# Kernel tuning notes

Measured on AMD Instinct MI355X. Metric: run time of the kernel, lower is better.

## Reference

```python
import jax, jax.numpy as jnp
import numpy as np

D = 64       # embedding_dim
N = 10000    # nodes
E = 160000   # edges (avg degree 16)
R = 16       # removals
C = 512      # connected edges scored per removal


def setup_inputs() -> dict:
    key = jax.random.key(0)
    ks = jax.random.split(key, 18)
    coords = jax.random.normal(ks[0], (N, 2), jnp.float32)
    edge_src = jax.random.randint(ks[1], (E,), 0, N, jnp.int32)
    edge_dst = jax.random.randint(ks[2], (E,), 0, N, jnp.int32)
    removal_idx = jax.random.randint(ks[3], (R,), 0, N, jnp.int32)
    conn_eidx = jax.random.randint(ks[4], (R, C), 0, E, jnp.int32)
    s2 = 1.0 / np.sqrt(2.0)
    sD = 1.0 / np.sqrt(D)
    s2D = 1.0 / np.sqrt(2 * D)
    return {
        "coords": coords,
        "W_emb": jax.random.normal(ks[5], (2, D), jnp.float32) * s2,
        "b_emb": jnp.zeros((D,), jnp.float32),
        "W_self0": jax.random.normal(ks[6], (D, D), jnp.float32) * sD,
        "W_neigh0": jax.random.normal(ks[7], (D, D), jnp.float32) * sD,
        "b_gnn0": jnp.zeros((D,), jnp.float32),
        "W_self1": jax.random.normal(ks[8], (D, D), jnp.float32) * sD,
        "W_neigh1": jax.random.normal(ks[9], (D, D), jnp.float32) * sD,
        "b_gnn1": jnp.zeros((D,), jnp.float32),
        "W_edge": jax.random.normal(ks[10], (2 * D, D), jnp.float32) * s2D,
        "b_edge": jnp.zeros((D,), jnp.float32),
        "W_score": jax.random.normal(ks[11], (2 * D, 1), jnp.float32) * s2D,
        "b_score": jnp.zeros((1,), jnp.float32),
        "edge_src": edge_src,
        "edge_dst": edge_dst,
        "removal_idx": removal_idx,
        "conn_eidx": conn_eidx,
    }


def reference(coords, W_emb, b_emb, W_self0, W_neigh0, b_gnn0,
              W_self1, W_neigh1, b_gnn1, W_edge, b_edge, W_score, b_score,
              edge_src, edge_dst, removal_idx, conn_eidx):
    Nn = coords.shape[0]
    h0 = coords @ W_emb + b_emb  # [N, D] init node embedding

    def gnn_layer(h, emask, Ws, Wn, b):
        # masked mean aggregation of neighbor messages, then linear + relu
        msg = h[edge_src] * emask[:, None]                       # [E, D]
        agg = jax.ops.segment_sum(msg, edge_dst, num_segments=Nn)
        deg = jax.ops.segment_sum(emask, edge_dst, num_segments=Nn)
        agg = agg / jnp.maximum(deg, 1.0)[:, None]
        return jax.nn.relu(h @ Ws + agg @ Wn + b)

    def per_removal(r, conn):
        # tempDestroy: mask out removed node's participation in message passing
        nmask = jnp.ones((Nn,), coords.dtype).at[r].set(0.0)
        emask = nmask[edge_src] * nmask[edge_dst]                # [E]
        h = h0
        h = gnn_layer(h, emask, W_self0, W_neigh0, b_gnn0) + h   # residual
        h = gnn_layer(h, emask, W_self1, W_neigh1, b_gnn1) + h
        s, d = edge_src[conn], edge_dst[conn]                    # connected edges
        ef = jax.nn.relu(jnp.concatenate([h[s], h[d]], -1) @ W_edge + b_edge)  # [C, D]
        r_embed = coords[r] @ W_emb + b_emb                      # [D]
        score_in = jnp.concatenate(
            [jnp.broadcast_to(r_embed, (conn.shape[0], r_embed.shape[0])), ef], -1)
        score = score_in @ W_score + b_score                     # [C, 1]
        return jax.nn.softmax(score, axis=0)[:, 0]               # softmax over edges

    return jax.vmap(per_removal)(removal_idx, conn_eidx)         # [R, C]
```

## Files before the change

### kernel.cpp

```cpp
#include <hip/hip_runtime.h>

#define Df 64
#define NN 10000
#define EE 160000
#define RR 16
#define CC 512
#define CAP1 128
#define CAP2 2048
#define BST 128
#define NGEMM 157
#define NAGG 2500
#define NEDG 625
#define NSLF 40
#define ND1B 512
#define ND2B 8192

__device__ float g_h0[NN * Df];
__device__ float g_h1b[NN * Df];
__device__ float g_h2b[NN * Df];
__device__ float g_agg[NN * Df];
__device__ float g_zrow[Df];
__device__ __align__(16) float g_W20[128 * Df];
__device__ __align__(16) float g_W21[128 * Df];
__device__ int g_deg[NN];
__device__ __align__(16) int g_bkt[NN * BST];
__device__ int g_m1mask[NN], g_m2mask[NN];
__device__ int g_mark1[RR][NN], g_mark2[RR][NN];
__device__ int g_n1[RR], g_n2[RR];
__device__ int g_list1[RR][CAP1], g_list2[RR][CAP2];
__device__ float g_d1[RR][CAP1][Df];
__device__ float g_d2[RR][CAP2][Df];
__device__ float g_score[RR * CC];

__device__ void compact256(const int* __restrict__ maskArr, int bit,
                           int* mark, int* list, int* nout, int cap) {
    int t = threadIdx.x;
    int lane = t & 63, wv = t >> 6;
    const int PER = 40;
    int base = t * PER;
    int loc = 0;
    for (int k = 0; k < PER; k++) { int v = base + k; if (v < NN) loc += (maskArr[v] >> bit) & 1; }
    int sc = loc;
#pragma unroll
    for (int off = 1; off < 64; off <<= 1) { int x = __shfl_up(sc, off, 64); if (lane >= off) sc += x; }
    __shared__ int wsumC[4];
    if (lane == 63) wsumC[wv] = sc;
    __syncthreads();
    if (t == 0) { int a = 0; for (int w2 = 0; w2 < 4; w2++) { int x = wsumC[w2]; wsumC[w2] = a; a += x; } }
    __syncthreads();
    int run = wsumC[wv] + (sc - loc);
    for (int k = 0; k < PER; k++) {
        int v = base + k;
        if (v < NN) {
            int f = (maskArr[v] >> bit) & 1;
            if (f && run < cap) { list[run] = v; mark[v] = run + 1; }
            else mark[v] = 0;
            run += f;
        }
    }
    if (t == 255) *nout = (run < cap) ? run : cap;
    __syncthreads();
}

__device__ void agg8(const float* __restrict__ hin, int b, int tid) {
    int lane = tid & 63, w = tid >> 6;
    int n = b * 4 + w;
    int deg = g_deg[n];
    int dg = deg < BST ? deg : BST;
    const int* bp = &g_bkt[n * BST];
    float s0 = 0.f, s1 = 0.f, s2 = 0.f, s3 = 0.f;
    float s4 = 0.f, s5 = 0.f, s6 = 0.f, s7 = 0.f;
    int i = 0;
    for (; i + 8 <= dg; i += 8) {
        int4 a = *(const int4*)&bp[i];
        int4 c = *(const int4*)&bp[i + 4];
        s0 += hin[a.x * Df + lane];
        s1 += hin[a.y * Df + lane];
        s2 += hin[a.z * Df + lane];
        s3 += hin[a.w * Df + lane];
        s4 += hin[c.x * Df + lane];
        s5 += hin[c.y * Df + lane];
        s6 += hin[c.z * Df + lane];
        s7 += hin[c.w * Df + lane];
    }
    for (; i < dg; i++) s0 += hin[bp[i] * Df + lane];
    float s = ((s0 + s1) + (s2 + s3)) + ((s4 + s5) + (s6 + s7));
    g_agg[n * Df + lane] = s / fmaxf((float)deg, 1.f);
}

__device__ void gemm_tile(const float* __restrict__ hin, float* __restrict__ hout,
                          const float* __restrict__ W2, const float* __restrict__ bias,
                          int m0, int tid, char* smem) {
    float (*Xs)[68] = (float(*)[68])smem;
    float (*Wl)[64] = (float(*)[64])(smem + 8704);
    int tx = tid & 15, ty = tid >> 4;
    float acc[4][4];
#pragma unroll
    for (int i = 0; i < 4; i++)
#pragma unroll
        for (int j = 0; j < 4; j++) acc[i][j] = 0.f;

    for (int c = 0; c < 4; c++) {
        const float* src = (c < 2) ? hin : g_agg;
        int kb = (c & 1) * 32;
        int kbase = c * 32;
#pragma unroll
        for (int rep = 0; rep < 2; rep++) {
            int slot = tid + rep * 256;
            int m = slot >> 3, q = slot & 7;
            int n = m0 + m;
            float4 v = make_float4(0.f, 0.f, 0.f, 0.f);
            if (n < NN) v = *(const float4*)&src[n * Df + kb + q * 4];
            Xs[q * 4 + 0][m] = v.x; Xs[q * 4 + 1][m] = v.y;
            Xs[q * 4 + 2][m] = v.z; Xs[q * 4 + 3][m] = v.w;
            int k = slot >> 4, dq = slot & 15;
            *(float4*)&Wl[k][dq * 4] = *(const float4*)&W2[(kbase + k) * Df + dq * 4];
        }
        __syncthreads();
#pragma unroll
        for (int k = 0; k < 32; k++) {
            float4 x4 = *(const float4*)&Xs[k][ty * 4];
            float4 w4 = *(const float4*)&Wl[k][tx * 4];
            float xs[4] = {x4.x, x4.y, x4.z, x4.w};
            float ws[4] = {w4.x, w4.y, w4.z, w4.w};
#pragma unroll
            for (int i = 0; i < 4; i++)
#pragma unroll
                for (int j = 0; j < 4; j++) acc[i][j] += xs[i] * ws[j];
        }
        __syncthreads();
    }
    float4 b4 = *(const float4*)&bias[tx * 4];
    float bb[4] = {b4.x, b4.y, b4.z, b4.w};
#pragma unroll
    for (int i = 0; i < 4; i++) {
        int n = m0 + ty * 4 + i;
        if (n < NN) {
            float4 hv = *(const float4*)&hin[n * Df + tx * 4];
            float4 o;
            o.x = fmaxf(acc[i][0] + bb[0], 0.f) + hv.x;
            o.y = fmaxf(acc[i][1] + bb[1], 0.f) + hv.y;
            o.z = fmaxf(acc[i][2] + bb[2], 0.f) + hv.z;
            o.w = fmaxf(acc[i][3] + bb[3], 0.f) + hv.w;
            *(float4*)&hout[n * Df + tx * 4] = o;
        }
    }
}

__device__ void delta1_blk(int rel, int tid, const int* __restrict__ removal,
                           const float* __restrict__ Ws, const float* __restrict__ Wn,
                           const float* __restrict__ bias, char* smem) {
    float* s_h = (float*)smem;
    float* s_a = s_h + 4 * Df;
    int ri = rel >> 5, y = rel & 31;
    int lane = tid & 63, w = tid >> 6;
    int j = y * 4 + w;
    if (j >= g_n1[ri]) return;
    int v = g_list1[ri][j];
    int r = removal[ri];
    float p0s = 0.f, p1s = 0.f, p2s = 0.f, p3s = 0.f; int cnt = 0;
    if (v != r) {
        int deg = g_deg[v];
        int dg = deg < BST ? deg : BST;
        const int* bp = &g_bkt[v * BST];
        int i = 0;
        for (; i + 4 <= dg; i += 4) {
            int c0 = bp[i], c1 = bp[i + 1], c2 = bp[i + 2], c3 = bp[i + 3];
            const float* p0 = (c0 == r) ? g_zrow : &g_h0[c0 * Df];
            const float* p1 = (c1 == r) ? g_zrow : &g_h0[c1 * Df];
            const float* p2 = (c2 == r) ? g_zrow : &g_h0[c2 * Df];
            const float* p3 = (c3 == r) ? g_zrow : &g_h0[c3 * Df];
            p0s += p0[lane]; p1s += p1[lane]; p2s += p2[lane]; p3s += p3[lane];
            cnt += (c0 != r) + (c1 != r) + (c2 != r) + (c3 != r);
        }
        for (; i < dg; i++) {
            int c = bp[i];
            const float* p = (c == r) ? g_zrow : &g_h0[c * Df];
            p0s += p[lane]; cnt += (c != r);
        }
    }
    float aggd = (p0s + p1s) + (p2s + p3s);
    float hv = g_h0[v * Df + lane];
    s_h[w * Df + lane] = hv;
    s_a[w * Df + lane] = aggd / fmaxf((float)cnt, 1.f);
    float acc = bias[lane];
#pragma unroll 16
    for (int k = 0; k < Df; k++)
        acc += s_h[w * Df + k] * Ws[k * Df + lane] + s_a[w * Df + k] * Wn[k * Df + lane];
    g_d1[ri][j][lane] = fmaxf(acc, 0.f) + hv;
}

__device__ void delta2_blk(int rel, int tid, const int* __restrict__ removal,
                           const float* __restrict__ Ws, const float* __restrict__ Wn,
                           const float* __restrict__ bias, char* smem) {
    float* s_h = (float*)smem;
    float* s_a = s_h + 4 * Df;
    int ri = rel >> 9, y = rel & 511;
    int lane = tid & 63, w = tid >> 6;
    int j = y * 4 + w;
    if (j >= g_n2[ri]) return;
    int v = g_list2[ri][j];
    int r = removal[ri];
    const int* mk1 = g_mark1[ri];
    float p0s = 0.f, p1s = 0.f, p2s = 0.f, p3s = 0.f; int cnt = 0;
    if (v != r) {
        int deg = g_deg[v];
        int dg = deg < BST ? deg : BST;
        const int* bp = &g_bkt[v * BST];
        int i = 0;
        for (; i + 4 <= dg; i += 4) {
            int c0 = bp[i], c1 = bp[i + 1], c2 = bp[i + 2], c3 = bp[i + 3];
            int m0 = mk1[c0], m1 = mk1[c1], m2 = mk1[c2], m3 = mk1[c3];
            const float* p0 = (c0 == r) ? g_zrow : (m0 > 0 ? &g_d1[ri][m0 - 1][0] : &g_h1b[c0 * Df]);
            const float* p1 = (c1 == r) ? g_zrow : (m1 > 0 ? &g_d1[ri][m1 - 1][0] : &g_h1b[c1 * Df]);
            const float* p2 = (c2 == r) ? g_zrow : (m2 > 0 ? &g_d1[ri][m2 - 1][0] : &g_h1b[c2 * Df]);
            const float* p3 = (c3 == r) ? g_zrow : (m3 > 0 ? &g_d1[ri][m3 - 1][0] : &g_h1b[c3 * Df]);
            p0s += p0[lane]; p1s += p1[lane]; p2s += p2[lane]; p3s += p3[lane];
            cnt += (c0 != r) + (c1 != r) + (c2 != r) + (c3 != r);
        }
        for (; i < dg; i++) {
            int c = bp[i];
            int m = mk1[c];
            const float* p = (c == r) ? g_zrow : (m > 0 ? &g_d1[ri][m - 1][0] : &g_h1b[c * Df]);
            p0s += p[lane]; cnt += (c != r);
        }
    }
    float aggd = (p0s + p1s) + (p2s + p3s);
    int mv = mk1[v];
    float hv = (mv > 0) ? g_d1[ri][mv - 1][lane] : g_h1b[v * Df + lane];
    s_h[w * Df + lane] = hv;
    s_a[w * Df + lane] = aggd / fmaxf((float)cnt, 1.f);
    float acc = bias[lane];
#pragma unroll 16
    for (int k = 0; k < Df; k++)
        acc += s_h[w * Df + k] * Ws[k * Df + lane] + s_a[w * Df + k] * Wn[k * Df + lane];
    g_d2[ri][j][lane] = fmaxf(acc, 0.f) + hv;
}

__global__ void k_init(const float* __restrict__ coords, const float* __restrict__ We,
                       const float* __restrict__ be, const float* __restrict__ Ws0,
                       const float* __restrict__ Wn0, const float* __restrict__ Ws1,
                       const float* __restrict__ Wn1) {
    int i = blockIdx.x * 256 + threadIdx.x;
    if (i < NN * Df) {
        int n = i >> 6, d = i & 63;
        g_h0[i] = coords[2 * n] * We[d] + coords[2 * n + 1] * We[Df + d] + be[d];
    }
    if (i < NN) { g_deg[i] = 0; g_m1mask[i] = 0; g_m2mask[i] = 0; }
    if (i < Df) g_zrow[i] = 0.f;
    if (i < 8192) {
        int k = i >> 6, d = i & 63;
        g_W20[i] = (k < 64) ? Ws0[k * 64 + d] : Wn0[(k - 64) * 64 + d];
        g_W21[i] = (k < 64) ? Ws1[k * 64 + d] : Wn1[(k - 64) * 64 + d];
    }
}

__global__ void k_fillflag(const int* __restrict__ esrc, const int* __restrict__ edst,
                           const int* __restrict__ removal) {
    __shared__ int s_rem[RR];
    int tid = threadIdx.x;
    if (tid < RR) s_rem[tid] = removal[tid];
    __syncthreads();
    int e = blockIdx.x * 256 + tid;
    if (e < EE) {
        int s = esrc[e], d = edst[e];
        int p = atomicAdd(&g_deg[d], 1);
        if (p < BST) g_bkt[d * BST + p] = s;
        int m = 0;
#pragma unroll
        for (int ri = 0; ri < RR; ri++)
            if (s == s_rem[ri]) m |= (1 << ri);
        if (m) atomicOr(&g_m1mask[d], m);
    }
    if (blockIdx.x == 0 && tid < RR)
        atomicOr(&g_m1mask[removal[tid]], 1 << tid);
}

__global__ __launch_bounds__(256) void k_L3(const int* __restrict__ esrc,
                                            const int* __restrict__ edst) {
    int b = blockIdx.x, tid = threadIdx.x;
    if (b < NAGG) { agg8(g_h0, b, tid); return; }
    if (b < NAGG + NEDG) {
        int e = (b - NAGG) * 256 + tid;
        if (e < EE) {
            int m = g_m1mask[esrc[e]];
            if (m) atomicOr(&g_m2mask[edst[e]], m);
        }
        return;
    }
    if (b < NAGG + NEDG + NSLF) {
        int v = (b - NAGG - NEDG) * 256 + tid;
        if (v < NN) {
            int m = g_m1mask[v];
            if (m) atomicOr(&g_m2mask[v], m);
        }
        return;
    }
    int ri = b - NAGG - NEDG - NSLF;
    compact256(g_m1mask, ri, g_mark1[ri], g_list1[ri], &g_n1[ri], CAP1);
}

__global__ __launch_bounds__(256) void k_L4(const int* __restrict__ removal,
        const float* __restrict__ Ws0, const float* __restrict__ Wn0,
        const float* __restrict__ b0) {
    __shared__ __align__(16) char smem[16896];
    int b = blockIdx.x, tid = threadIdx.x;
    if (b < NGEMM) { gemm_tile(g_h0, g_h1b, g_W20, b0, b * 64, tid, smem); return; }
    if (b < NGEMM + ND1B) { delta1_blk(b - NGEMM, tid, removal, Ws0, Wn0, b0, smem); return; }
    int ri = b - NGEMM - ND1B;
    compact256(g_m2mask, ri, g_mark2[ri], g_list2[ri], &g_n2[ri], CAP2);
}

__global__ __launch_bounds__(256) void k_L5(const int* __restrict__ removal,
        const float* __restrict__ Ws1, const float* __restrict__ Wn1,
        const float* __restrict__ b1) {
    __shared__ __align__(16) char smem[2048];
    int b = blockIdx.x, tid = threadIdx.x;
    if (b < NAGG) { agg8(g_h1b, b, tid); return; }
    delta2_blk(b - NAGG, tid, removal, Ws1, Wn1, b1, smem);
}

__global__ __launch_bounds__(256) void k_gemm1(const float* __restrict__ b1) {
    __shared__ __align__(16) char smem[16896];
    gemm_tile(g_h1b, g_h2b, g_W21, b1, blockIdx.x * 64, threadIdx.x, smem);
}

__global__ __launch_bounds__(256) void k_score(const int* __restrict__ conn,
        const int* __restrict__ removal, const int* __restrict__ esrc,
        const int* __restrict__ edst, const float* __restrict__ We,
        const float* __restrict__ be, const float* __restrict__ Wsc,
        const float* __restrict__ bsc) {
    __shared__ const float* ptrs[128];
    __shared__ float Xs[32][68];
    __shared__ float Wl[32][64];
    __shared__ float su;
    int tid = threadIdx.x;
    int e0 = blockIdx.x * 64;
    int ri = e0 >> 9;

    if (tid < 64) {
        int e = conn[e0 + tid];
        int s = esrc[e], d = edst[e];
        int ms = g_mark2[ri][s], md = g_mark2[ri][d];
        ptrs[tid]      = (ms > 0) ? &g_d2[ri][ms - 1][0] : &g_h2b[s * Df];
        ptrs[64 + tid] = (md > 0) ? &g_d2[ri][md - 1][0] : &g_h2b[d * Df];
    } else if (tid < 128) {
        int lane = tid & 63;
        float up = g_h0[removal[ri] * Df + lane] * Wsc[lane];
#pragma unroll
        for (int off = 32; off > 0; off >>= 1) up += __shfl_xor(up, off, 64);
        if (lane == 0) su = up;
    }
    __syncthreads();

    int tx = tid & 15, ty = tid >> 4;
    float acc[4][4];
#pragma unroll
    for (int i = 0; i < 4; i++)
#pragma unroll
        for (int j = 0; j < 4; j++) acc[i][j] = 0.f;

    for (int c = 0; c < 4; c++) {
        int kb = (c & 1) * 32;
#pragma unroll
        for (int rep = 0; rep < 2; rep++) {
            int slot = tid + rep * 256;
            int m = slot >> 3, q = slot & 7;
            const float* p = ((c < 2) ? ptrs[m] : ptrs[64 + m]) + kb + q * 4;
            float4 v = *(const float4*)p;
            Xs[q * 4 + 0][m] = v.x; Xs[q * 4 + 1][m] = v.y;
            Xs[q * 4 + 2][m] = v.z; Xs[q * 4 + 3][m] = v.w;
            int k = slot >> 4, dq = slot & 15;
            *(float4*)&Wl[k][dq * 4] = *(const float4*)&We[(c * 32 + k) * Df + dq * 4];
        }
        __syncthreads();
#pragma unroll
        for (int k = 0; k < 32; k++) {
            float4 x4 = *(const float4*)&Xs[k][ty * 4];
            float4 w4 = *(const float4*)&Wl[k][tx * 4];
            float xs[4] = {x4.x, x4.y, x4.z, x4.w};
            float ws[4] = {w4.x, w4.y, w4.z, w4.w};
#pragma unroll
            for (int i = 0; i < 4; i++)
#pragma unroll
                for (int j = 0; j < 4; j++) acc[i][j] += xs[i] * ws[j];
        }
        __syncthreads();
    }

    float4 be4 = *(const float4*)&be[tx * 4];
    float4 w2  = *(const float4*)&Wsc[Df + tx * 4];
    float bb[4] = {be4.x, be4.y, be4.z, be4.w};
    float ww[4] = {w2.x, w2.y, w2.z, w2.w};
    float sb = su + bsc[0];
#pragma unroll
    for (int i = 0; i < 4; i++) {
        float part = 0.f;
#pragma unroll
        for (int j = 0; j < 4; j++) part += fmaxf(acc[i][j] + bb[j], 0.f) * ww[j];
#pragma unroll
        for (int off = 1; off < 16; off <<= 1) part += __shfl_xor(part, off, 64);
        if (tx == 0) g_score[e0 + ty * 4 + i] = part + sb;
    }
}

__global__ void k_softmax(float* __restrict__ out) {
    int r = blockIdx.x;
    int t = threadIdx.x;
    float v0 = g_score[r * CC + t];
    float v1 = g_score[r * CC + 256 + t];
    __shared__ float red[256];
    red[t] = fmaxf(v0, v1);
    __syncthreads();
    for (int off = 128; off > 0; off >>= 1) {
        if (t < off) red[t] = fmaxf(red[t], red[t + off]);
        __syncthreads();
    }
    float mx = red[0];
    __syncthreads();
    float e0 = expf(v0 - mx), e1 = expf(v1 - mx);
    red[t] = e0 + e1;
    __syncthreads();
    for (int off = 128; off > 0; off >>= 1) {
        if (t < off) red[t] += red[t + off];
        __syncthreads();
    }
    float inv = 1.f / red[0];
    out[r * CC + t] = e0 * inv;
    out[r * CC + 256 + t] = e1 * inv;
}

extern "C" void kernel_launch(void* const* d_in, const int* in_sizes, int n_in,
                              void* d_out, int out_size, void* d_ws, size_t ws_size,
                              hipStream_t stream) {
    const float* coords   = (const float*)d_in[0];
    const float* W_emb    = (const float*)d_in[1];
    const float* b_emb    = (const float*)d_in[2];
    const float* W_self0  = (const float*)d_in[3];
    const float* W_neigh0 = (const float*)d_in[4];
    const float* b_gnn0   = (const float*)d_in[5];
    const float* W_self1  = (const float*)d_in[6];
    const float* W_neigh1 = (const float*)d_in[7];
    const float* b_gnn1   = (const float*)d_in[8];
    const float* W_edge   = (const float*)d_in[9];
    const float* b_edge   = (const float*)d_in[10];
    const float* W_score  = (const float*)d_in[11];
    const float* b_score  = (const float*)d_in[12];
    const int* esrc       = (const int*)d_in[13];
    const int* edst       = (const int*)d_in[14];
    const int* removal    = (const int*)d_in[15];
    const int* conn       = (const int*)d_in[16];

    k_init<<<2500, 256, 0, stream>>>(coords, W_emb, b_emb, W_self0, W_neigh0,
                                     W_self1, W_neigh1);
    k_fillflag<<<NEDG, 256, 0, stream>>>(esrc, edst, removal);
    k_L3<<<NAGG + NEDG + NSLF + RR, 256, 0, stream>>>(esrc, edst);
    k_L4<<<NGEMM + ND1B + RR, 256, 0, stream>>>(removal, W_self0, W_neigh0, b_gnn0);
    k_L5<<<NAGG + ND2B, 256, 0, stream>>>(removal, W_self1, W_neigh1, b_gnn1);
    k_gemm1<<<NGEMM, 256, 0, stream>>>(b_gnn1);
    k_score<<<RR * CC / 64, 256, 0, stream>>>(conn, removal, esrc, edst,
                                              W_edge, b_edge, W_score, b_score);
    k_softmax<<<RR, 256, 0, stream>>>((float*)d_out);
}
```

Measured before the change: 126.7 us.

## Fuse neighbor aggregation into GEMM tiles and softmax into score kernel

The separate neighbor-mean aggregation blocks and the g_agg buffer are gone. Each GEMM tile now gathers its own 64 rows of aggregated neighbors into shared memory before the matmul, which also removes the standalone second-layer GEMM launch. Softmax is folded into the score kernel with a last-block-done atomic counter per removal, dropping two launches. The trade-off is fewer GEMM blocks doing the serial gather work (157 instead of 2500) and larger shared memory per block, which may lower occupancy for the delta blocks that share those kernels.

```diff
diff --git a/kernel.cpp b/kernel.cpp
--- a/kernel.cpp
+++ b/kernel.cpp
@@ -9,7 +9,6 @@
 #define CAP2 2048
 #define BST 128
 #define NGEMM 157
-#define NAGG 2500
 #define NEDG 625
 #define NSLF 40
 #define ND1B 512
@@ -18,7 +17,6 @@
 __device__ float g_h0[NN * Df];
 __device__ float g_h1b[NN * Df];
 __device__ float g_h2b[NN * Df];
-__device__ float g_agg[NN * Df];
 __device__ float g_zrow[Df];
 __device__ __align__(16) float g_W20[128 * Df];
 __device__ __align__(16) float g_W21[128 * Df];
@@ -31,6 +29,7 @@
 __device__ float g_d1[RR][CAP1][Df];
 __device__ float g_d2[RR][CAP2][Df];
 __device__ float g_score[RR * CC];
+__device__ int g_scnt[RR];
 
 __device__ void compact256(const int* __restrict__ maskArr, int bit,
                            int* mark, int* list, int* nout, int cap) {
@@ -62,37 +61,41 @@
     __syncthreads();
 }
 
-__device__ void agg8(const float* __restrict__ hin, int b, int tid) {
-    int lane = tid & 63, w = tid >> 6;
-    int n = b * 4 + w;
-    int deg = g_deg[n];
-    int dg = deg < BST ? deg : BST;
-    const int* bp = &g_bkt[n * BST];
-    float s0 = 0.f, s1 = 0.f, s2 = 0.f, s3 = 0.f;
-    float s4 = 0.f, s5 = 0.f, s6 = 0.f, s7 = 0.f;
-    int i = 0;
-    for (; i + 8 <= dg; i += 8) {
-        int4 a = *(const int4*)&bp[i];
-        int4 c = *(const int4*)&bp[i + 4];
-        s0 += hin[a.x * Df + lane];
-        s1 += hin[a.y * Df + lane];
-        s2 += hin[a.z * Df + lane];
-        s3 += hin[a.w * Df + lane];
-        s4 += hin[c.x * Df + lane];
-        s5 += hin[c.y * Df + lane];
-        s6 += hin[c.z * Df + lane];
-        s7 += hin[c.w * Df + lane];
-    }
-    for (; i < dg; i++) s0 += hin[bp[i] * Df + lane];
-    float s = ((s0 + s1) + (s2 + s3)) + ((s4 + s5) + (s6 + s7));
-    g_agg[n * Df + lane] = s / fmaxf((float)deg, 1.f);
-}
-
-__device__ void gemm_tile(const float* __restrict__ hin, float* __restrict__ hout,
-                          const float* __restrict__ W2, const float* __restrict__ bias,
-                          int m0, int tid, char* smem) {
+__device__ void gemm_agg_tile(const float* __restrict__ hin, float* __restrict__ hout,
+                              const float* __restrict__ W2, const float* __restrict__ bias,
+                              int m0, int tid, char* smem) {
     float (*Xs)[68] = (float(*)[68])smem;
     float (*Wl)[64] = (float(*)[64])(smem + 8704);
+    float* AgT = (float*)(smem + 8704 + 8192);
+    int lane = tid & 63, w = tid >> 6;
+
+    for (int i = 0; i < 16; i++) {
+        int m = w * 16 + i;
+        int n = m0 + m;
+        float res = 0.f;
+        if (n < NN) {
+            int deg = g_deg[n];
+            int dg = deg < BST ? deg : BST;
+            const int* bp = &g_bkt[n * BST];
+            float s0 = 0.f, s1 = 0.f, s2 = 0.f, s3 = 0.f;
+            float s4 = 0.f, s5 = 0.f, s6 = 0.f, s7 = 0.f;
+            int ii = 0;
+            for (; ii + 8 <= dg; ii += 8) {
+                int4 a = *(const int4*)&bp[ii];
+                int4 c4 = *(const int4*)&bp[ii + 4];
+                s0 += hin[a.x * Df + lane];  s1 += hin[a.y * Df + lane];
+                s2 += hin[a.z * Df + lane];  s3 += hin[a.w * Df + lane];
+                s4 += hin[c4.x * Df + lane]; s5 += hin[c4.y * Df + lane];
+                s6 += hin[c4.z * Df + lane]; s7 += hin[c4.w * Df + lane];
+            }
+            for (; ii < dg; ii++) s0 += hin[bp[ii] * Df + lane];
+            res = (((s0 + s1) + (s2 + s3)) + ((s4 + s5) + (s6 + s7)))
+                  / fmaxf((float)deg, 1.f);
+        }
+        AgT[lane * 68 + m] = res;
+    }
+    __syncthreads();
+
     int tx = tid & 15, ty = tid >> 4;
     float acc[4][4];
 #pragma unroll
@@ -101,25 +104,35 @@
         for (int j = 0; j < 4; j++) acc[i][j] = 0.f;
 
     for (int c = 0; c < 4; c++) {
-        const float* src = (c < 2) ? hin : g_agg;
-        int kb = (c & 1) * 32;
         int kbase = c * 32;
-#pragma unroll
-        for (int rep = 0; rep < 2; rep++) {
-            int slot = tid + rep * 256;
-            int m = slot >> 3, q = slot & 7;
-            int n = m0 + m;
-            float4 v = make_float4(0.f, 0.f, 0.f, 0.f);
-            if (n < NN) v = *(const float4*)&src[n * Df + kb + q * 4];
-            Xs[q * 4 + 0][m] = v.x; Xs[q * 4 + 1][m] = v.y;
-            Xs[q * 4 + 2][m] = v.z; Xs[q * 4 + 3][m] = v.w;
-            int k = slot >> 4, dq = slot & 15;
-            *(float4*)&Wl[k][dq * 4] = *(const float4*)&W2[(kbase + k) * Df + dq * 4];
-        }
-        __syncthreads();
+        if (c < 2) {
+            int kb = c * 32;
+#pragma unroll
+            for (int rep = 0; rep < 2; rep++) {
+                int slot = tid + rep * 256;
+                int m = slot >> 3, q = slot & 7;
+                int n = m0 + m;
+                float4 v = make_float4(0.f, 0.f, 0.f, 0.f);
+                if (n < NN) v = *(const float4*)&hin[n * Df + kb + q * 4];
+                Xs[q * 4 + 0][m] = v.x; Xs[q * 4 + 1][m] = v.y;
+                Xs[q * 4 + 2][m] = v.z; Xs[q * 4 + 3][m] = v.w;
+                int k = slot >> 4, dq = slot & 15;
+                *(float4*)&Wl[k][dq * 4] = *(const float4*)&W2[(kbase + k) * Df + dq * 4];
+            }
+        } else {
+#pragma unroll
+            for (int rep = 0; rep < 2; rep++) {
+                int slot = tid + rep * 256;
+                int k = slot >> 4, dq = slot & 15;
+                *(float4*)&Wl[k][dq * 4] = *(const float4*)&W2[(kbase + k) * Df + dq * 4];
+            }
+        }
+        __syncthreads();
+        int ks0 = (c - 2) * 32;
 #pragma unroll
         for (int k = 0; k < 32; k++) {
-            float4 x4 = *(const float4*)&Xs[k][ty * 4];
+            float4 x4 = (c < 2) ? *(const float4*)&Xs[k][ty * 4]
+                                : *(const float4*)&AgT[(ks0 + k) * 68 + ty * 4];
             float4 w4 = *(const float4*)&Wl[k][tx * 4];
             float xs[4] = {x4.x, x4.y, x4.z, x4.w};
             float ws[4] = {w4.x, w4.y, w4.z, w4.w};
@@ -248,6 +261,7 @@
     }
     if (i < NN) { g_deg[i] = 0; g_m1mask[i] = 0; g_m2mask[i] = 0; }
     if (i < Df) g_zrow[i] = 0.f;
+    if (i < RR) g_scnt[i] = 0;
     if (i < 8192) {
         int k = i >> 6, d = i & 63;
         g_W20[i] = (k < 64) ? Ws0[k * 64 + d] : Wn0[(k - 64) * 64 + d];
@@ -279,61 +293,59 @@
 __global__ __launch_bounds__(256) void k_L3(const int* __restrict__ esrc,
                                             const int* __restrict__ edst) {
     int b = blockIdx.x, tid = threadIdx.x;
-    if (b < NAGG) { agg8(g_h0, b, tid); return; }
-    if (b < NAGG + NEDG) {
-        int e = (b - NAGG) * 256 + tid;
+    if (b < RR) {
+        compact256(g_m1mask, b, g_mark1[b], g_list1[b], &g_n1[b], CAP1);
+        return;
+    }
+    if (b < RR + NEDG) {
+        int e = (b - RR) * 256 + tid;
         if (e < EE) {
             int m = g_m1mask[esrc[e]];
             if (m) atomicOr(&g_m2mask[edst[e]], m);
         }
         return;
     }
-    if (b < NAGG + NEDG + NSLF) {
-        int v = (b - NAGG - NEDG) * 256 + tid;
-        if (v < NN) {
-            int m = g_m1mask[v];
-            if (m) atomicOr(&g_m2mask[v], m);
-        }
-        return;
-    }
-    int ri = b - NAGG - NEDG - NSLF;
-    compact256(g_m1mask, ri, g_mark1[ri], g_list1[ri], &g_n1[ri], CAP1);
+    int v = (b - RR - NEDG) * 256 + tid;
+    if (v < NN) {
+        int m = g_m1mask[v];
+        if (m) atomicOr(&g_m2mask[v], m);
+    }
 }
 
 __global__ __launch_bounds__(256) void k_L4(const int* __restrict__ removal,
         const float* __restrict__ Ws0, const float* __restrict__ Wn0,
         const float* __restrict__ b0) {
-    __shared__ __align__(16) char smem[16896];
+    __shared__ __align__(16) char smem[34304];
     int b = blockIdx.x, tid = threadIdx.x;
-    if (b < NGEMM) { gemm_tile(g_h0, g_h1b, g_W20, b0, b * 64, tid, smem); return; }
-    if (b < NGEMM + ND1B) { delta1_blk(b - NGEMM, tid, removal, Ws0, Wn0, b0, smem); return; }
-    int ri = b - NGEMM - ND1B;
-    compact256(g_m2mask, ri, g_mark2[ri], g_list2[ri], &g_n2[ri], CAP2);
+    if (b < NGEMM) { gemm_agg_tile(g_h0, g_h1b, g_W20, b0, b * 64, tid, smem); return; }
+    if (b < NGEMM + RR) {
+        int ri = b - NGEMM;
+        compact256(g_m2mask, ri, g_mark2[ri], g_list2[ri], &g_n2[ri], CAP2);
+        return;
+    }
+    delta1_blk(b - NGEMM - RR, tid, removal, Ws0, Wn0, b0, smem);
 }
 
 __global__ __launch_bounds__(256) void k_L5(const int* __restrict__ removal,
         const float* __restrict__ Ws1, const float* __restrict__ Wn1,
         const float* __restrict__ b1) {
-    __shared__ __align__(16) char smem[2048];
+    __shared__ __align__(16) char smem[34304];
     int b = blockIdx.x, tid = threadIdx.x;
-    if (b < NAGG) { agg8(g_h1b, b, tid); return; }
-    delta2_blk(b - NAGG, tid, removal, Ws1, Wn1, b1, smem);
-}
-
-__global__ __launch_bounds__(256) void k_gemm1(const float* __restrict__ b1) {
-    __shared__ __align__(16) char smem[16896];
-    gemm_tile(g_h1b, g_h2b, g_W21, b1, blockIdx.x * 64, threadIdx.x, smem);
-}
-
-__global__ __launch_bounds__(256) void k_score(const int* __restrict__ conn,
+    if (b < NGEMM) { gemm_agg_tile(g_h1b, g_h2b, g_W21, b1, b * 64, tid, smem); return; }
+    delta2_blk(b - NGEMM, tid, removal, Ws1, Wn1, b1, smem);
+}
+
+__global__ __launch_bounds__(256) void k_scoreSM(const int* __restrict__ conn,
         const int* __restrict__ removal, const int* __restrict__ esrc,
         const int* __restrict__ edst, const float* __restrict__ We,
         const float* __restrict__ be, const float* __restrict__ Wsc,
-        const float* __restrict__ bsc) {
-    __shared__ const float* ptrs[128];
-    __shared__ float Xs[32][68];
-    __shared__ float Wl[32][64];
-    __shared__ float su;
+        const float* __restrict__ bsc, float* __restrict__ out) {
+    __shared__ __align__(16) char smem[18064];
+    const float** ptrs = (const float**)smem;
+    float (*Xs)[68] = (float(*)[68])(smem + 1024);
+    float (*Wl)[64] = (float(*)[64])(smem + 1024 + 8704);
+    float* su = (float*)(smem + 1024 + 8704 + 8192);
+    __shared__ int s_last;
     int tid = threadIdx.x;
     int e0 = blockIdx.x * 64;
     int ri = e0 >> 9;
@@ -349,7 +361,7 @@
         float up = g_h0[removal[ri] * Df + lane] * Wsc[lane];
 #pragma unroll
         for (int off = 32; off > 0; off >>= 1) up += __shfl_xor(up, off, 64);
-        if (lane == 0) su = up;
+        if (lane == 0) *su = up;
     }
     __syncthreads();
 
@@ -392,7 +404,7 @@
     float4 w2  = *(const float4*)&Wsc[Df + tx * 4];
     float bb[4] = {be4.x, be4.y, be4.z, be4.w};
     float ww[4] = {w2.x, w2.y, w2.z, w2.w};
-    float sb = su + bsc[0];
+    float sb = *su + bsc[0];
 #pragma unroll
     for (int i = 0; i < 4; i++) {
         float part = 0.f;
@@ -400,34 +412,43 @@
         for (int j = 0; j < 4; j++) part += fmaxf(acc[i][j] + bb[j], 0.f) * ww[j];
 #pragma unroll
         for (int off = 1; off < 16; off <<= 1) part += __shfl_xor(part, off, 64);
-        if (tx == 0) g_score[e0 + ty * 4 + i] = part + sb;
-    }
-}
-
-__global__ void k_softmax(float* __restrict__ out) {
-    int r = blockIdx.x;
-    int t = threadIdx.x;
-    float v0 = g_score[r * CC + t];
-    float v1 = g_score[r * CC + 256 + t];
-    __shared__ float red[256];
-    red[t] = fmaxf(v0, v1);
+        if (tx == 0)
+            __hip_atomic_store(&g_score[e0 + ty * 4 + i], part + sb,
+                               __ATOMIC_RELEASE, __HIP_MEMORY_SCOPE_AGENT);
+    }
+
+    __syncthreads();
+    if (tid == 0) {
+        int old = __hip_atomic_fetch_add(&g_scnt[ri], 1,
+                                         __ATOMIC_ACQ_REL, __HIP_MEMORY_SCOPE_AGENT);
+        s_last = (old == (CC / 64 - 1));
+    }
+    __syncthreads();
+    if (!s_last) return;
+
+    float* red = (float*)smem;
+    float v0 = __hip_atomic_load(&g_score[ri * CC + tid],
+                                 __ATOMIC_ACQUIRE, __HIP_MEMORY_SCOPE_AGENT);
+    float v1 = __hip_atomic_load(&g_score[ri * CC + 256 + tid],
+                                 __ATOMIC_ACQUIRE, __HIP_MEMORY_SCOPE_AGENT);
+    red[tid] = fmaxf(v0, v1);
     __syncthreads();
     for (int off = 128; off > 0; off >>= 1) {
-        if (t < off) red[t] = fmaxf(red[t], red[t + off]);
+        if (tid < off) red[tid] = fmaxf(red[tid], red[tid + off]);
         __syncthreads();
     }
     float mx = red[0];
     __syncthreads();
-    float e0 = expf(v0 - mx), e1 = expf(v1 - mx);
-    red[t] = e0 + e1;
+    float e0f = expf(v0 - mx), e1f = expf(v1 - mx);
+    red[tid] = e0f + e1f;
     __syncthreads();
     for (int off = 128; off > 0; off >>= 1) {
-        if (t < off) red[t] += red[t + off];
+        if (tid < off) red[tid] += red[tid + off];
         __syncthreads();
     }
     float inv = 1.f / red[0];
-    out[r * CC + t] = e0 * inv;
-    out[r * CC + 256 + t] = e1 * inv;
+    out[ri * CC + tid] = e0f * inv;
+    out[ri * CC + 256 + tid] = e1f * inv;
 }
 
 extern "C" void kernel_launch(void* const* d_in, const int* in_sizes, int n_in,
@@ -454,11 +475,10 @@
     k_init<<<2500, 256, 0, stream>>>(coords, W_emb, b_emb, W_self0, W_neigh0,
                                      W_self1, W_neigh1);
     k_fillflag<<<NEDG, 256, 0, stream>>>(esrc, edst, removal);
-    k_L3<<<NAGG + NEDG + NSLF + RR, 256, 0, stream>>>(esrc, edst);
-    k_L4<<<NGEMM + ND1B + RR, 256, 0, stream>>>(removal, W_self0, W_neigh0, b_gnn0);
-    k_L5<<<NAGG + ND2B, 256, 0, stream>>>(removal, W_self1, W_neigh1, b_gnn1);
-    k_gemm1<<<NGEMM, 256, 0, stream>>>(b_gnn1);
-    k_score<<<RR * CC / 64, 256, 0, stream>>>(conn, removal, esrc, edst,
-                                              W_edge, b_edge, W_score, b_score);
-    k_softmax<<<RR, 256, 0, stream>>>((float*)d_out);
-}
+    k_L3<<<RR + NEDG + NSLF, 256, 0, stream>>>(esrc, edst);
+    k_L4<<<NGEMM + RR + ND1B, 256, 0, stream>>>(removal, W_self0, W_neigh0, b_gnn0);
+    k_L5<<<NGEMM + ND2B, 256, 0, stream>>>(removal, W_self1, W_neigh1, b_gnn1);
+    k_scoreSM<<<RR * CC / 64, 256, 0, stream>>>(conn, removal, esrc, edst,
+                                                W_edge, b_edge, W_score, b_score,
+                                                (float*)d_out);
+}
```

Result: slower. 459.6 us (+262.6%).
